# Optimization experiments

Hardware: AMD Instinct MI355X
Metric: run time of the kernel (lower is better)

Reference implementation:

```python
import jax, jax.numpy as jnp
import numpy as np


def setup_inputs() -> dict:
    key = jax.random.key(0)
    kx, kq, kk, kv = jax.random.split(key, 4)
    B, C, H, W = 4, 512, 64, 64
    CK = C // 8  # low-rank q/k dim
    x = jax.random.normal(kx, (B, C, H, W), dtype=jnp.float32)
    # 1x1 conv weights (spectral-normed at runtime in torch; here plain params,
    # same math: a [out,in] matmul over the flattened spatial dim)
    s = 1.0 / np.sqrt(C)
    Wq = jax.random.normal(kq, (CK, C), dtype=jnp.float32) * s
    Wk = jax.random.normal(kk, (CK, C), dtype=jnp.float32) * s
    Wv = jax.random.normal(kv, (C, C), dtype=jnp.float32) * s
    gamma = jnp.zeros((1,), dtype=jnp.float32)
    return {"x": x, "Wq": Wq, "Wk": Wk, "Wv": Wv, "gamma": gamma}


def reference(x, Wq, Wk, Wv, gamma):
    B, C, H, W = x.shape
    N = H * W
    xf = x.reshape(B, C, N)                         # [B,C,N]
    f = jnp.einsum('kc,bcn->bkn', Wq, xf)           # [B,C/8,N]
    g = jnp.einsum('kc,bcn->bkn', Wk, xf)           # [B,C/8,N]
    h = jnp.einsum('oc,bcn->bon', Wv, xf)           # [B,C,N]
    # scores[b,i,j] = sum_k f[b,k,i] * g[b,k,j]; softmax over dim=1 (i axis)
    scores = jnp.einsum('bki,bkj->bij', f, g)       # [B,N,N]
    beta = jax.nn.softmax(scores, axis=1)
    # o[b,c,j] = sum_i h[b,c,i] * beta[b,i,j]
    o = gamma * jnp.einsum('bci,bij->bcj', h, beta) + xf
    pooled = jnp.mean(o, axis=2).reshape(B, C, 1, 1)  # adaptive_avg_pool2d(.,1)
    return pooled, beta
```

## Files before the change

kernel.cpp:

```cpp
#include <hip/hip_runtime.h>

constexpr int N  = 4096;
constexpr int C  = 512;
constexpr int CK = 64;
constexpr int B  = 4;

typedef __attribute__((ext_vector_type(8))) short short8;
typedef __attribute__((ext_vector_type(4))) float f32x4;

__global__ __launch_bounds__(256, 2)
void proj_fg(const float* __restrict__ x, const float* __restrict__ Wq,
             const float* __restrict__ Wk, float* __restrict__ fg)
{
    int b  = blockIdx.y;
    int i0 = blockIdx.x * 64;
    __shared__ __align__(16) float xs[16][64];
    __shared__ __align__(16) float ws[16][132];
    int tid = threadIdx.x, ty = tid >> 4, tx = tid & 15;
    float acc[8][4] = {};
    const float* xb = x + (size_t)b * C * N;

    for (int c0 = 0; c0 < C; c0 += 16) {
        {
            int cc = tid >> 4, col4 = (tid & 15) * 4;
            *(float4*)&xs[cc][col4] =
                *(const float4*)&xb[(size_t)(c0 + cc) * N + i0 + col4];
        }
        for (int v = tid; v < 2048; v += 256) {
            int row = v >> 4, cc = v & 15;
            ws[cc][row] = (row < 64) ? Wq[row * C + c0 + cc]
                                     : Wk[(row - 64) * C + c0 + cc];
        }
        __syncthreads();
        #pragma unroll
        for (int cc = 0; cc < 16; ++cc) {
            float4 wa = *(const float4*)&ws[cc][ty * 4];
            float4 wb = *(const float4*)&ws[cc][64 + ty * 4];
            float4 xa = *(const float4*)&xs[cc][tx * 4];
            float wr[8] = {wa.x, wa.y, wa.z, wa.w, wb.x, wb.y, wb.z, wb.w};
            float xc[4] = {xa.x, xa.y, xa.z, xa.w};
            #pragma unroll
            for (int r = 0; r < 8; ++r)
                #pragma unroll
                for (int cl = 0; cl < 4; ++cl)
                    acc[r][cl] += wr[r] * xc[cl];
        }
        __syncthreads();
    }
    float* outb = fg + (size_t)b * 128 * N;
    #pragma unroll
    for (int r = 0; r < 8; ++r) {
        int row = (r < 4) ? (ty * 4 + r) : (64 + ty * 4 + (r - 4));
        *(float4*)&outb[(size_t)row * N + i0 + tx * 4] =
            make_float4(acc[r][0], acc[r][1], acc[r][2], acc[r][3]);
    }
}

__global__ __launch_bounds__(256)
void transpose_split(const float* __restrict__ fg,
                     ushort* __restrict__ fT_hi, ushort* __restrict__ fT_lo,
                     ushort* __restrict__ gT_hi, ushort* __restrict__ gT_lo)
{
    int b = blockIdx.z, half = blockIdx.y, i0 = blockIdx.x * 64;
    const float* src = fg + ((size_t)b * 128 + half * 64) * N;
    __shared__ float tile[64][68];
    int t = threadIdx.x;
    {
        int k = t >> 2, ic = (t & 3) * 16;
        #pragma unroll
        for (int c4 = 0; c4 < 16; c4 += 4)
            *(float4*)&tile[k][ic + c4] =
                *(const float4*)&src[(size_t)k * N + i0 + ic + c4];
    }
    __syncthreads();
    int i = t >> 2, kc = (t & 3) * 16;
    ushort hi[16], lo[16];
    #pragma unroll
    for (int kk = 0; kk < 16; ++kk) {
        float v = tile[kc + kk][i];
        unsigned bits = __float_as_uint(v);
        unsigned hb   = bits & 0xFFFF0000u;
        hi[kk] = (ushort)(hb >> 16);
        float lof = v - __uint_as_float(hb);
        lo[kk] = (ushort)(__float_as_uint(lof) >> 16);
    }
    size_t ofs = ((size_t)b * N + i0 + i) * 64 + kc;
    ushort* dh = (half ? gT_hi : fT_hi) + ofs;
    ushort* dl = (half ? gT_lo : fT_lo) + ofs;
    ((uint4*)dh)[0] = ((uint4*)hi)[0]; ((uint4*)dh)[1] = ((uint4*)hi)[1];
    ((uint4*)dl)[0] = ((uint4*)lo)[0]; ((uint4*)dl)[1] = ((uint4*)lo)[1];
}

template <int PASS>
__global__ __launch_bounds__(256, 2)
void scores_pass(const ushort* __restrict__ fT_hi, const ushort* __restrict__ fT_lo,
                 const ushort* __restrict__ gT_hi, const ushort* __restrict__ gT_lo,
                 const float* __restrict__ inv_l, float* __restrict__ colsum,
                 float* __restrict__ beta, float* __restrict__ rowsum)
{
    int b = blockIdx.z, i0 = blockIdx.y * 128, j0 = blockIdx.x * 128;
    __shared__ ushort sm[4][128][72];
    int tid = threadIdx.x;

    const ushort* fh = fT_hi + ((size_t)b * N + i0) * 64;
    const ushort* fl = fT_lo + ((size_t)b * N + i0) * 64;
    const ushort* gh = gT_hi + ((size_t)b * N + j0) * 64;
    const ushort* gl = gT_lo + ((size_t)b * N + j0) * 64;
    #pragma unroll
    for (int v = tid; v < 1024; v += 256) {
        int row = v >> 3, ch = (v & 7) * 8;
        *(uint4*)&sm[0][row][ch] = *(const uint4*)&fh[(size_t)row * 64 + ch];
        *(uint4*)&sm[1][row][ch] = *(const uint4*)&fl[(size_t)row * 64 + ch];
        *(uint4*)&sm[2][row][ch] = *(const uint4*)&gh[(size_t)row * 64 + ch];
        *(uint4*)&sm[3][row][ch] = *(const uint4*)&gl[(size_t)row * 64 + ch];
    }
    __syncthreads();

    int w = tid >> 6, lane = tid & 63, l15 = lane & 15, quad = lane >> 4;
    f32x4 acc[2][8] = {};

    const int pA[3] = {0, 0, 1};
    const int pB[3] = {2, 3, 2};
    #pragma unroll
    for (int p = 0; p < 3; ++p) {
        #pragma unroll
        for (int ks = 0; ks < 2; ++ks) {
            int kofs = ks * 32 + quad * 8;
            short8 afr[2];
            #pragma unroll
            for (int tr = 0; tr < 2; ++tr)
                afr[tr] = *(const short8*)&sm[pA[p]][w * 32 + tr * 16 + l15][kofs];
            #pragma unroll
            for (int tc = 0; tc < 8; ++tc) {
                short8 bfr = *(const short8*)&sm[pB[p]][tc * 16 + l15][kofs];
                acc[0][tc] = __builtin_amdgcn_mfma_f32_16x16x32_bf16(afr[0], bfr, acc[0][tc], 0, 0, 0);
                acc[1][tc] = __builtin_amdgcn_mfma_f32_16x16x32_bf16(afr[1], bfr, acc[1][tc], 0, 0, 0);
            }
        }
    }

    if (PASS == 1) {
        float cs[8];
        #pragma unroll
        for (int tc = 0; tc < 8; ++tc) cs[tc] = 0.f;
        #pragma unroll
        for (int tr = 0; tr < 2; ++tr)
            #pragma unroll
            for (int tc = 0; tc < 8; ++tc)
                #pragma unroll
                for (int r = 0; r < 4; ++r)
                    cs[tc] += __expf(acc[tr][tc][r] - 20.0f);
        __syncthreads();
        float* red = (float*)&sm[0][0][0];
        #pragma unroll
        for (int tc = 0; tc < 8; ++tc)
            red[(tc * 16 + l15) * 17 + (w * 4 + quad)] = cs[tc];
        __syncthreads();
        if (tid < 128) {
            float s = 0.f;
            #pragma unroll
            for (int sl = 0; sl < 16; ++sl) s += red[tid * 17 + sl];
            atomicAdd(&colsum[(size_t)b * N + j0 + tid], s);
        }
    } else {
        float il[8];
        #pragma unroll
        for (int tc = 0; tc < 8; ++tc)
            il[tc] = inv_l[(size_t)b * N + j0 + tc * 16 + l15];
        float* pb = beta + (size_t)b * N * N;
        #pragma unroll
        for (int tr = 0; tr < 2; ++tr) {
            float rp[4] = {0.f, 0.f, 0.f, 0.f};
            #pragma unroll
            for (int tc = 0; tc < 8; ++tc) {
                int j = j0 + tc * 16 + l15;
                #pragma unroll
                for (int r = 0; r < 4; ++r) {
                    int i = i0 + w * 32 + tr * 16 + quad * 4 + r;
                    float v = __expf(acc[tr][tc][r] - 20.0f) * il[tc];
                    rp[r] += v;
                    pb[(size_t)i * N + j] = v;
                }
            }
            #pragma unroll
            for (int r = 0; r < 4; ++r) {
                float s = rp[r];
                s += __shfl_xor(s, 1); s += __shfl_xor(s, 2);
                s += __shfl_xor(s, 4); s += __shfl_xor(s, 8);
                if (l15 == 0)
                    atomicAdd(&rowsum[(size_t)b * N + i0 + w * 32 + tr * 16 + quad * 4 + r], s);
            }
        }
    }
}

__global__ __launch_bounds__(256)
void invert_colsum(float* __restrict__ c)
{
    int t = blockIdx.x * 256 + threadIdx.x;
    c[t] = 1.0f / c[t];
}

__global__ __launch_bounds__(256)
void reduce_xr(const float* __restrict__ x, const float* __restrict__ rowsum,
               float* __restrict__ meanx, float* __restrict__ tvec)
{
    int b = blockIdx.y, c = blockIdx.x, tid = threadIdx.x;
    const float* xr = x + ((size_t)b * C + c) * N;
    const float* rr = rowsum + (size_t)b * N;
    float sx = 0.f, st = 0.f;
    for (int base = 0; base < N; base += 1024) {
        int i = base + tid * 4;
        float4 xv = *(const float4*)&xr[i];
        float4 rv = *(const float4*)&rr[i];
        sx += xv.x + xv.y + xv.z + xv.w;
        st += xv.x * rv.x + xv.y * rv.y + xv.z * rv.z + xv.w * rv.w;
    }
    __shared__ float s1[256], s2[256];
    s1[tid] = sx; s2[tid] = st;
    __syncthreads();
    for (int s = 128; s > 0; s >>= 1) {
        if (tid < s) { s1[tid] += s1[tid + s]; s2[tid] += s2[tid + s]; }
        __syncthreads();
    }
    if (tid == 0) {
        meanx[b * C + c] = s1[0] * (1.0f / N);
        tvec [b * C + c] = s2[0];
    }
}

__global__ __launch_bounds__(64)
void pooled_out(const float* __restrict__ Wv, const float* __restrict__ meanx,
                const float* __restrict__ tvec, const float* __restrict__ gamma,
                float* __restrict__ out)
{
    int b = blockIdx.y, c = blockIdx.x;
    const float* wr = Wv + (size_t)c * C;
    const float* t  = tvec + (size_t)b * C;
    float s = 0.f;
    for (int cc = threadIdx.x; cc < C; cc += 64) s += wr[cc] * t[cc];
    for (int off = 32; off > 0; off >>= 1) s += __shfl_down(s, off);
    if (threadIdx.x == 0)
        out[b * C + c] = meanx[b * C + c] + gamma[0] * (1.0f / N) * s;
}

extern "C" void kernel_launch(void* const* d_in, const int* in_sizes, int n_in,
                              void* d_out, int out_size, void* d_ws, size_t ws_size,
                              hipStream_t stream)
{
    const float* x     = (const float*)d_in[0];
    const float* Wq    = (const float*)d_in[1];
    const float* Wk    = (const float*)d_in[2];
    const float* Wv    = (const float*)d_in[3];
    const float* gamma = (const float*)d_in[4];
    float* out  = (float*)d_out;
    float* beta = out + (size_t)B * C;

    float*  fg    = (float*)d_ws;
    ushort* ubase = (ushort*)(fg + (size_t)B * 128 * N);
    ushort* fT_hi = ubase;
    ushort* fT_lo = fT_hi + (size_t)B * N * 64;
    ushort* gT_hi = fT_lo + (size_t)B * N * 64;
    ushort* gT_lo = gT_hi + (size_t)B * N * 64;
    float*  colsum = (float*)(gT_lo + (size_t)B * N * 64);
    float*  rowsum = colsum + (size_t)B * N;
    float*  meanx  = rowsum + (size_t)B * N;
    float*  tvec   = meanx + (size_t)B * C;

    hipMemsetAsync(colsum, 0, 2 * (size_t)B * N * sizeof(float), stream);

    proj_fg        <<<dim3(N / 64, B),           256, 0, stream>>>(x, Wq, Wk, fg);
    transpose_split<<<dim3(N / 64, 2, B),        256, 0, stream>>>(fg, fT_hi, fT_lo, gT_hi, gT_lo);
    scores_pass<1> <<<dim3(N / 128, N / 128, B), 256, 0, stream>>>(fT_hi, fT_lo, gT_hi, gT_lo,
                                                                   colsum, colsum, beta, rowsum);
    invert_colsum  <<<dim3(B * N / 256),         256, 0, stream>>>(colsum);
    scores_pass<2> <<<dim3(N / 128, N / 128, B), 256, 0, stream>>>(fT_hi, fT_lo, gT_hi, gT_lo,
                                                                   colsum, colsum, beta, rowsum);
    reduce_xr      <<<dim3(C, B),                256, 0, stream>>>(x, rowsum, meanx, tvec);
    pooled_out     <<<dim3(C, B),                 64, 0, stream>>>(Wv, meanx, tvec, gamma, out);
}
```

Measured before the change: 481.7 us.

## Fuse f/g projection with transpose and bf16 hi/lo split; reorder MFMA loop

The projection kernel now runs 512 threads per block, each computing a 4x4 tile. It converts its outputs to bf16 hi/lo pairs, transposes them through shared memory and writes fT/gT directly. This removes the separate transpose_split kernel and the fp32 fg round trip through global memory. The scores kernel's three-pass MFMA loop is also restructured so hi and lo fragments are loaded once per k-step and the three products are issued back to back. This should cut LDS reloads, at the cost of extra live registers and more shared memory in the projection kernel.

```diff
diff --git a/kernel.cpp b/kernel.cpp
--- a/kernel.cpp
+++ b/kernel.cpp
@@ -8,25 +8,30 @@
 typedef __attribute__((ext_vector_type(8))) short short8;
 typedef __attribute__((ext_vector_type(4))) float f32x4;
 
-__global__ __launch_bounds__(256, 2)
-void proj_fg(const float* __restrict__ x, const float* __restrict__ Wq,
-             const float* __restrict__ Wk, float* __restrict__ fg)
+__global__ __launch_bounds__(512, 1)
+void proj_fgT(const float* __restrict__ x, const float* __restrict__ Wq,
+              const float* __restrict__ Wk,
+              ushort* __restrict__ fT_hi, ushort* __restrict__ fT_lo,
+              ushort* __restrict__ gT_hi, ushort* __restrict__ gT_lo)
 {
     int b  = blockIdx.y;
     int i0 = blockIdx.x * 64;
-    __shared__ __align__(16) float xs[16][64];
-    __shared__ __align__(16) float ws[16][132];
+    __shared__ __align__(16) float  xs[16][64];
+    __shared__ __align__(16) float  ws[16][132];
+    __shared__ __align__(16) ushort oh[64][136];
+    __shared__ __align__(16) ushort ol[64][136];
     int tid = threadIdx.x, ty = tid >> 4, tx = tid & 15;
-    float acc[8][4] = {};
+    float acc[4][4] = {};
     const float* xb = x + (size_t)b * C * N;
 
     for (int c0 = 0; c0 < C; c0 += 16) {
-        {
+        if (tid < 256) {
             int cc = tid >> 4, col4 = (tid & 15) * 4;
             *(float4*)&xs[cc][col4] =
                 *(const float4*)&xb[(size_t)(c0 + cc) * N + i0 + col4];
         }
-        for (int v = tid; v < 2048; v += 256) {
+        #pragma unroll
+        for (int v = tid; v < 2048; v += 512) {
             int row = v >> 4, cc = v & 15;
             ws[cc][row] = (row < 64) ? Wq[row * C + c0 + cc]
                                      : Wk[(row - 64) * C + c0 + cc];
@@ -35,60 +40,37 @@
         #pragma unroll
         for (int cc = 0; cc < 16; ++cc) {
             float4 wa = *(const float4*)&ws[cc][ty * 4];
-            float4 wb = *(const float4*)&ws[cc][64 + ty * 4];
             float4 xa = *(const float4*)&xs[cc][tx * 4];
-            float wr[8] = {wa.x, wa.y, wa.z, wa.w, wb.x, wb.y, wb.z, wb.w};
+            float wr[4] = {wa.x, wa.y, wa.z, wa.w};
             float xc[4] = {xa.x, xa.y, xa.z, xa.w};
             #pragma unroll
-            for (int r = 0; r < 8; ++r)
+            for (int r = 0; r < 4; ++r)
                 #pragma unroll
                 for (int cl = 0; cl < 4; ++cl)
                     acc[r][cl] += wr[r] * xc[cl];
         }
         __syncthreads();
     }
-    float* outb = fg + (size_t)b * 128 * N;
+
     #pragma unroll
-    for (int r = 0; r < 8; ++r) {
-        int row = (r < 4) ? (ty * 4 + r) : (64 + ty * 4 + (r - 4));
-        *(float4*)&outb[(size_t)row * N + i0 + tx * 4] =
-            make_float4(acc[r][0], acc[r][1], acc[r][2], acc[r][3]);
-    }
-}
-
-__global__ __launch_bounds__(256)
-void transpose_split(const float* __restrict__ fg,
-                     ushort* __restrict__ fT_hi, ushort* __restrict__ fT_lo,
-                     ushort* __restrict__ gT_hi, ushort* __restrict__ gT_lo)
-{
-    int b = blockIdx.z, half = blockIdx.y, i0 = blockIdx.x * 64;
-    const float* src = fg + ((size_t)b * 128 + half * 64) * N;
-    __shared__ float tile[64][68];
-    int t = threadIdx.x;
-    {
-        int k = t >> 2, ic = (t & 3) * 16;
-        #pragma unroll
-        for (int c4 = 0; c4 < 16; c4 += 4)
-            *(float4*)&tile[k][ic + c4] =
-                *(const float4*)&src[(size_t)k * N + i0 + ic + c4];
-    }
+    for (int r = 0; r < 4; ++r)
+        #pragma unroll
+        for (int cl = 0; cl < 4; ++cl) {
+            float v = acc[r][cl];
+            unsigned bits = __float_as_uint(v);
+            unsigned hb   = bits & 0xFFFF0000u;
+            float lof = v - __uint_as_float(hb);
+            oh[tx * 4 + cl][ty * 4 + r] = (ushort)(hb >> 16);
+            ol[tx * 4 + cl][ty * 4 + r] = (ushort)(__float_as_uint(lof) >> 16);
+        }
     __syncthreads();
-    int i = t >> 2, kc = (t & 3) * 16;
-    ushort hi[16], lo[16];
-    #pragma unroll
-    for (int kk = 0; kk < 16; ++kk) {
-        float v = tile[kc + kk][i];
-        unsigned bits = __float_as_uint(v);
-        unsigned hb   = bits & 0xFFFF0000u;
-        hi[kk] = (ushort)(hb >> 16);
-        float lof = v - __uint_as_float(hb);
-        lo[kk] = (ushort)(__float_as_uint(lof) >> 16);
-    }
+
+    int i = tid >> 3, kc = (tid & 7) * 8;
     size_t ofs = ((size_t)b * N + i0 + i) * 64 + kc;
-    ushort* dh = (half ? gT_hi : fT_hi) + ofs;
-    ushort* dl = (half ? gT_lo : fT_lo) + ofs;
-    ((uint4*)dh)[0] = ((uint4*)hi)[0]; ((uint4*)dh)[1] = ((uint4*)hi)[1];
-    ((uint4*)dl)[0] = ((uint4*)lo)[0]; ((uint4*)dl)[1] = ((uint4*)lo)[1];
+    *(uint4*)&fT_hi[ofs] = *(const uint4*)&oh[i][kc];
+    *(uint4*)&fT_lo[ofs] = *(const uint4*)&ol[i][kc];
+    *(uint4*)&gT_hi[ofs] = *(const uint4*)&oh[i][64 + kc];
+    *(uint4*)&gT_lo[ofs] = *(const uint4*)&ol[i][64 + kc];
 }
 
 template <int PASS>
@@ -119,22 +101,24 @@
     int w = tid >> 6, lane = tid & 63, l15 = lane & 15, quad = lane >> 4;
     f32x4 acc[2][8] = {};
 
-    const int pA[3] = {0, 0, 1};
-    const int pB[3] = {2, 3, 2};
     #pragma unroll
-    for (int p = 0; p < 3; ++p) {
-        #pragma unroll
-        for (int ks = 0; ks < 2; ++ks) {
-            int kofs = ks * 32 + quad * 8;
-            short8 afr[2];
-            #pragma unroll
-            for (int tr = 0; tr < 2; ++tr)
-                afr[tr] = *(const short8*)&sm[pA[p]][w * 32 + tr * 16 + l15][kofs];
-            #pragma unroll
-            for (int tc = 0; tc < 8; ++tc) {
-                short8 bfr = *(const short8*)&sm[pB[p]][tc * 16 + l15][kofs];
-                acc[0][tc] = __builtin_amdgcn_mfma_f32_16x16x32_bf16(afr[0], bfr, acc[0][tc], 0, 0, 0);
-                acc[1][tc] = __builtin_amdgcn_mfma_f32_16x16x32_bf16(afr[1], bfr, acc[1][tc], 0, 0, 0);
+    for (int ks = 0; ks < 2; ++ks) {
+        int kofs = ks * 32 + quad * 8;
+        short8 a_hi[2], a_lo[2];
+        #pragma unroll
+        for (int tr = 0; tr < 2; ++tr) {
+            a_hi[tr] = *(const short8*)&sm[0][w * 32 + tr * 16 + l15][kofs];
+            a_lo[tr] = *(const short8*)&sm[1][w * 32 + tr * 16 + l15][kofs];
+        }
+        #pragma unroll
+        for (int tc = 0; tc < 8; ++tc) {
+            short8 b_hi = *(const short8*)&sm[2][tc * 16 + l15][kofs];
+            short8 b_lo = *(const short8*)&sm[3][tc * 16 + l15][kofs];
+            #pragma unroll
+            for (int tr = 0; tr < 2; ++tr) {
+                acc[tr][tc] = __builtin_amdgcn_mfma_f32_16x16x32_bf16(a_hi[tr], b_hi, acc[tr][tc], 0, 0, 0);
+                acc[tr][tc] = __builtin_amdgcn_mfma_f32_16x16x32_bf16(a_hi[tr], b_lo, acc[tr][tc], 0, 0, 0);
+                acc[tr][tc] = __builtin_amdgcn_mfma_f32_16x16x32_bf16(a_lo[tr], b_hi, acc[tr][tc], 0, 0, 0);
             }
         }
     }
@@ -256,9 +240,7 @@
     float* out  = (float*)d_out;
     float* beta = out + (size_t)B * C;
 
-    float*  fg    = (float*)d_ws;
-    ushort* ubase = (ushort*)(fg + (size_t)B * 128 * N);
-    ushort* fT_hi = ubase;
+    ushort* fT_hi = (ushort*)d_ws;
     ushort* fT_lo = fT_hi + (size_t)B * N * 64;
     ushort* gT_hi = fT_lo + (size_t)B * N * 64;
     ushort* gT_lo = gT_hi + (size_t)B * N * 64;
@@ -269,8 +251,7 @@
 
     hipMemsetAsync(colsum, 0, 2 * (size_t)B * N * sizeof(float), stream);
 
-    proj_fg        <<<dim3(N / 64, B),           256, 0, stream>>>(x, Wq, Wk, fg);
-    transpose_split<<<dim3(N / 64, 2, B),        256, 0, stream>>>(fg, fT_hi, fT_lo, gT_hi, gT_lo);
+    proj_fgT       <<<dim3(N / 64, B),           512, 0, stream>>>(x, Wq, Wk, fT_hi, fT_lo, gT_hi, gT_lo);
     scores_pass<1> <<<dim3(N / 128, N / 128, B), 256, 0, stream>>>(fT_hi, fT_lo, gT_hi, gT_lo,
                                                                    colsum, colsum, beta, rowsum);
     invert_colsum  <<<dim3(B * N / 256),         256, 0, stream>>>(colsum);
```

Result: faster. 424.7 us (-11.8%).
